# Performance work log

Hardware: AMD Instinct MI355X
Metric: run time of the kernel (lower is better)

The kernel has to match this reference:

```python
import jax, jax.numpy as jnp
import numpy as np

B, L, E = 4, 1024, 1024
H = 16
HD = E // H
CLIP = 16
SCALE = 1.0 / np.sqrt(HD)


def setup_inputs() -> dict:
    key = jax.random.key(0)
    ks = jax.random.split(key, 13)
    def lin(k, fan_in, fan_out, gain):
        # xavier_uniform
        limit = gain * np.sqrt(6.0 / (fan_in + fan_out))
        return jax.random.uniform(k, (fan_out, fan_in), jnp.float32, -limit, limit)
    inv_sqrt2 = 1.0 / np.sqrt(2.0)
    return {
        "query": jax.random.normal(ks[0], (B, L, E), jnp.float32),
        "key": jax.random.normal(ks[1], (B, L, E), jnp.float32),
        "value": jax.random.normal(ks[2], (B, L, E), jnp.float32),
        "wq": lin(ks[3], E, E, inv_sqrt2), "bq": jnp.zeros((E,), jnp.float32),
        "wk": lin(ks[4], E, E, inv_sqrt2), "bk": jnp.zeros((E,), jnp.float32),
        "wv": lin(ks[5], E, E, inv_sqrt2), "bv": jnp.zeros((E,), jnp.float32),
        "wo": lin(ks[6], E, E, 1.0), "bo": jnp.zeros((E,), jnp.float32),
        "rel_k": jax.random.normal(ks[7], (2 * CLIP + 1, HD), jnp.float32) * 0.02,
        "rel_v": jax.random.normal(ks[8], (2 * CLIP + 1, HD), jnp.float32) * 0.02,
    }


def _heads(x):  # (B, L, E) -> (B, H, L, HD)
    return x.reshape(B, L, H, HD).transpose(0, 2, 1, 3)


def reference(query, key, value, wq, bq, wk, bk, wv, bv, wo, bo, rel_k, rel_v):
    q = _heads(query @ wq.T + bq)
    k = _heads(key @ wk.T + bk)
    v = _heads(value @ wv.T + bv)

    # relative-position index matrix (L_q, L_k), clipped to [-CLIP, CLIP]
    pos = jnp.arange(L)
    dist = jnp.clip(pos[None, :] - pos[:, None], -CLIP, CLIP) + CLIP
    r_k = rel_k[dist]  # (L, L, HD)
    r_v = rel_v[dist]  # (L, L, HD)

    dot = jnp.einsum('bhid,bhjd->bhij', q, k)
    rel = jnp.einsum('bhid,ijd->bhij', q, r_k)
    scores = (dot + rel) * SCALE
    attn = jax.nn.softmax(scores, axis=-1)

    y = jnp.einsum('bhij,bhjd->bhid', attn, v) + jnp.einsum('bhij,ijd->bhid', attn, r_v)
    y = y.transpose(0, 2, 1, 3).reshape(B, L, E)
    return y @ wo.T + bo
```

## Files before the change

### kernel.cpp

```cpp
#include <hip/hip_runtime.h>

#define BB 4
#define LL 1024
#define EE 1024
#define HH 16
#define HD 64
#define NBUCKET 33
#define SCALE 0.125f
#define SC2 (0.125f * 1.44269504088896f)

typedef unsigned short u16;
using f32x4 = __attribute__((ext_vector_type(4))) float;
using s16x8 = __attribute__((ext_vector_type(8))) short;

__device__ __forceinline__ u16 f2bf(float f) {
  union { float f; unsigned u; } x; x.f = f;
  unsigned r = (x.u + 0x7fffu + ((x.u >> 16) & 1u)) >> 16;
  return (u16)r;
}

__device__ __forceinline__ void gld_lds16(const void* g, void* s) {
  __builtin_amdgcn_global_load_lds((const __attribute__((address_space(1))) void*)g,
                                   (__attribute__((address_space(3))) void*)s, 16, 0, 0);
}

__global__ __launch_bounds__(256) void cvt_w(
    const float* __restrict__ wq, const float* __restrict__ wk, const float* __restrict__ wv,
    const float* __restrict__ wo, const float* __restrict__ rk,
    u16* __restrict__ owq, u16* __restrict__ owk, u16* __restrict__ owv,
    u16* __restrict__ owo, u16* __restrict__ ork) {
  const int bid = blockIdx.x;
  const int tid = threadIdx.x;
  if (bid < 4096) {
    const int z = bid >> 10;
    const int i = (bid & 1023) * 256 + tid;
    const float* in = z == 0 ? wq : (z == 1 ? wk : (z == 2 ? wv : wo));
    u16* out = z == 0 ? owq : (z == 1 ? owk : (z == 2 ? owv : owo));
    float4 f = ((const float4*)in)[i];
    ushort4 o;
    o.x = f2bf(f.x); o.y = f2bf(f.y); o.z = f2bf(f.z); o.w = f2bf(f.w);
    ((ushort4*)out)[i] = o;
  } else {
    const int i = (bid - 4096) * 256 + tid;
    ork[i] = (i < 33 * 64) ? f2bf(rk[i]) : (u16)0;
  }
}

template <int MODE>
__device__ __forceinline__ void gemm128_f32a(const float* __restrict__ A,
                                             const u16* __restrict__ Bw,
                                             const float* __restrict__ bias,
                                             u16* __restrict__ obf,
                                             int M, int N, int K, int m0, int n0) {
  __shared__ u16 a_sm[128 * 64];
  __shared__ u16 b_sm[128 * 64];
  const int tid = threadIdx.x;
  const int wave = tid >> 6, lane = tid & 63;
  const int row16 = lane & 15, quad = lane >> 4;
  const int wr = (wave >> 1) * 64, wc = (wave & 1) * 64;
  const int srow = lane >> 3, scol = (lane & 7) * 8;

  f32x4 acc[4][4] = {};

  for (int k0 = 0; k0 < K; k0 += 64) {
#pragma unroll
    for (int t = 0; t < 4; ++t) {
      const int chunk = wave * 4 + t;
      const int r = chunk * 8 + srow;
      gld_lds16(Bw + (size_t)(n0 + r) * K + k0 + scol, b_sm + chunk * 512);
    }
#pragma unroll
    for (int p = 0; p < 4; ++p) {
      const int pc = p * 256 + tid;
      const int r = pc >> 3, c0 = (pc & 7) * 8;
      const float4* src = (const float4*)(A + (size_t)(m0 + r) * K + k0 + c0);
      const float4 f0 = src[0], f1 = src[1];
      unsigned w0, w1, w2, w3;
      asm("v_cvt_pk_bf16_f32 %0, %1, %2" : "=v"(w0) : "v"(f0.x), "v"(f0.y));
      asm("v_cvt_pk_bf16_f32 %0, %1, %2" : "=v"(w1) : "v"(f0.z), "v"(f0.w));
      asm("v_cvt_pk_bf16_f32 %0, %1, %2" : "=v"(w2) : "v"(f1.x), "v"(f1.y));
      asm("v_cvt_pk_bf16_f32 %0, %1, %2" : "=v"(w3) : "v"(f1.z), "v"(f1.w));
      union { unsigned u[4]; s16x8 v; } w;
      w.u[0] = w0; w.u[1] = w1; w.u[2] = w2; w.u[3] = w3;
      *(s16x8*)&a_sm[r * 64 + c0] = w.v;
    }
    __syncthreads();
#pragma unroll
    for (int ks = 0; ks < 2; ++ks) {
      s16x8 af[4], bf[4];
#pragma unroll
      for (int mi = 0; mi < 4; ++mi)
        af[mi] = *(const s16x8*)&a_sm[(wr + mi * 16 + row16) * 64 + ks * 32 + quad * 8];
#pragma unroll
      for (int ni = 0; ni < 4; ++ni)
        bf[ni] = *(const s16x8*)&b_sm[(wc + ni * 16 + row16) * 64 + ks * 32 + quad * 8];
#pragma unroll
      for (int mi = 0; mi < 4; ++mi)
#pragma unroll
        for (int ni = 0; ni < 4; ++ni)
          acc[mi][ni] = __builtin_amdgcn_mfma_f32_16x16x32_bf16(af[mi], bf[ni], acc[mi][ni], 0, 0, 0);
    }
    __syncthreads();
  }

#pragma unroll
  for (int mi = 0; mi < 4; ++mi)
#pragma unroll
    for (int ni = 0; ni < 4; ++ni) {
      const int n = n0 + wc + ni * 16 + row16;
      const float bn = bias[n];
      if (MODE == 2) {
        const int mr0 = m0 + wr + mi * 16 + quad * 4;
        const int b = mr0 >> 10, l = mr0 & 1023;
        const int h = n >> 6, hd = n & 63;
        ushort4 o;
        o.x = f2bf(acc[mi][ni][0] + bn);
        o.y = f2bf(acc[mi][ni][1] + bn);
        o.z = f2bf(acc[mi][ni][2] + bn);
        o.w = f2bf(acc[mi][ni][3] + bn);
        *(ushort4*)&obf[((size_t)((b * HH + h) * HD + hd)) * LL + l] = o;
      } else {
#pragma unroll
        for (int r = 0; r < 4; ++r) {
          const int m = m0 + wr + mi * 16 + quad * 4 + r;
          const float v = acc[mi][ni][r] + bn;
          const int b = m >> 10, l = m & 1023, h = n >> 6, hd = n & 63;
          obf[((size_t)((b * HH + h) * LL + l)) * HD + hd] = f2bf(v);
        }
      }
    }
}

__device__ __forceinline__ void gemm128_bt_f32out(const u16* __restrict__ A,
                                                  const u16* __restrict__ Bw,
                                                  const float* __restrict__ bias,
                                                  float* __restrict__ ofp,
                                                  int M, int N, int K, int m0, int n0) {
  __shared__ u16 a_sm[128 * 64];
  __shared__ u16 b_sm[128 * 64];
  const int tid = threadIdx.x;
  const int wave = tid >> 6, lane = tid & 63;
  const int row16 = lane & 15, quad = lane >> 4;
  const int wr = (wave >> 1) * 64, wc = (wave & 1) * 64;
  const int srow = lane >> 3, scol = (lane & 7) * 8;

  f32x4 acc[4][4] = {};

  for (int k0 = 0; k0 < K; k0 += 64) {
#pragma unroll
    for (int t = 0; t < 4; ++t) {
      const int chunk = wave * 4 + t;
      const int r = chunk * 8 + srow;
      gld_lds16(A + (size_t)(m0 + r) * K + k0 + scol, a_sm + chunk * 512);
      gld_lds16(Bw + (size_t)(n0 + r) * K + k0 + scol, b_sm + chunk * 512);
    }
    __syncthreads();
#pragma unroll
    for (int ks = 0; ks < 2; ++ks) {
      s16x8 af[4], bf[4];
#pragma unroll
      for (int mi = 0; mi < 4; ++mi)
        af[mi] = *(const s16x8*)&a_sm[(wr + mi * 16 + row16) * 64 + ks * 32 + quad * 8];
#pragma unroll
      for (int ni = 0; ni < 4; ++ni)
        bf[ni] = *(const s16x8*)&b_sm[(wc + ni * 16 + row16) * 64 + ks * 32 + quad * 8];
#pragma unroll
      for (int mi = 0; mi < 4; ++mi)
#pragma unroll
        for (int ni = 0; ni < 4; ++ni)
          acc[mi][ni] = __builtin_amdgcn_mfma_f32_16x16x32_bf16(af[mi], bf[ni], acc[mi][ni], 0, 0, 0);
    }
    __syncthreads();
  }

#pragma unroll
  for (int mi = 0; mi < 4; ++mi)
#pragma unroll
    for (int ni = 0; ni < 4; ++ni) {
      const int n = n0 + wc + ni * 16 + row16;
      const float bn = bias[n];
#pragma unroll
      for (int r = 0; r < 4; ++r) {
        const int m = m0 + wr + mi * 16 + quad * 4 + r;
        ofp[(size_t)m * N + n] = acc[mi][ni][r] + bn;
      }
    }
}

__global__ __launch_bounds__(256) void proj_gemm(
    const float* __restrict__ xq, const float* __restrict__ xk, const float* __restrict__ xv,
    const u16* __restrict__ wqb, const u16* __restrict__ wkb, const u16* __restrict__ wvb,
    const float* __restrict__ bq, const float* __restrict__ bk, const float* __restrict__ bv,
    u16* __restrict__ oq, u16* __restrict__ ok, u16* __restrict__ ovt) {
  if (blockIdx.z == 0)
    gemm128_f32a<0>(xq, wqb, bq, oq, BB * LL, EE, EE, blockIdx.y * 128, blockIdx.x * 128);
  else if (blockIdx.z == 1)
    gemm128_f32a<0>(xk, wkb, bk, ok, BB * LL, EE, EE, blockIdx.y * 128, blockIdx.x * 128);
  else
    gemm128_f32a<2>(xv, wvb, bv, ovt, BB * LL, EE, EE, blockIdx.y * 128, blockIdx.x * 128);
}

__global__ __launch_bounds__(256) void out_gemm(const u16* __restrict__ Y,
                                                const u16* __restrict__ wob,
                                                const float* __restrict__ bo,
                                                float* __restrict__ out) {
  gemm128_bt_f32out(Y, wob, bo, out, BB * LL, EE, EE, blockIdx.y * 128, blockIdx.x * 128);
}

__global__ __launch_bounds__(256) void attn_fused(
    const u16* __restrict__ Q, const u16* __restrict__ Kb, const u16* __restrict__ Vt,
    const u16* __restrict__ RKp, const float* __restrict__ RV, u16* __restrict__ Y) {
  __shared__ __align__(16) float qr_sm[4][576];
  __shared__ __align__(16) float s_sm[4][16 * 36];
  __shared__ __align__(16) unsigned char kv[16384];

  const int tid = threadIdx.x;
  const int wave = tid >> 6, lane = tid & 63;
  const int row16 = lane & 15, quad = lane >> 4;
  const int bh = blockIdx.x & 63;
  const int i0 = (blockIdx.x >> 6) * 64;
  const int wq0 = i0 + wave * 16;
  const u16* qp = Q + (size_t)bh * LL * HD;
  const char* kpB = (const char*)(Kb + (size_t)bh * LL * HD);
  const char* vpB = (const char*)(Vt + (size_t)bh * HD * LL);

  float* qr_w = &qr_sm[wave][0];
  float* s_w = &s_sm[wave][0];

  int srcK[2], srcV[2];
#pragma unroll
  for (int t = 0; t < 2; ++t) {
    const int cK = (wave * 2 + t) * 64 + lane;
    const int rw = cK >> 3;
    const int cb = ((cK * 16) & 127) ^ ((rw & 7) << 4);
    srcK[t] = rw * 128 + cb;
    srcV[t] = rw * 2048 + cb;
  }
  const int q2 = row16 >> 2;
  const int prow = ((((q2 << 1) | (q2 >> 1)) & 3) << 2) + (row16 & 3);
  const int swzK = (prow & 7) << 4;
  const int swzV = (row16 & 7) << 4;
  const int rho4 = (((quad << 1) | (quad >> 1)) & 3) << 2;

#pragma unroll
  for (int t = 0; t < 2; ++t) {
    gld_lds16(kpB + srcK[t], kv + (wave * 2 + t) * 1024);
    gld_lds16(vpB + srcV[t], kv + 8192 + (wave * 2 + t) * 1024);
  }

  for (int t = lane; t < 16 * 36; t += 64) s_w[t] = 0.f;

  s16x8 qf[2];
#pragma unroll
  for (int ks = 0; ks < 2; ++ks)
    qf[ks] = *(const s16x8*)(qp + (size_t)(wq0 + row16) * HD + ks * 32 + quad * 8);

  f32x4 a0, a2;
#pragma unroll
  for (int nt = 0; nt < 3; ++nt) {
    f32x4 a = {};
#pragma unroll
    for (int ks = 0; ks < 2; ++ks) {
      s16x8 afr = *(const s16x8*)(RKp + (size_t)(nt * 16 + row16) * HD + ks * 32 + quad * 8);
      a = __builtin_amdgcn_mfma_f32_16x16x32_bf16(afr, qf[ks], a, 0, 0, 0);
    }
    if (nt == 0) a0 = a;
    if (nt == 2) a2 = a;
#pragma unroll
    for (int r = 0; r < 4; ++r) {
      const int bk = nt * 16 + quad * 4 + r;
      if (bk < NBUCKET) qr_w[bk * 17 + row16] = a[r];
    }
  }
  const float blo = __shfl(a0[0], row16);
  const float bhi = __shfl(a2[0], row16);

  f32x4 oacc[4] = {};
  float rsum = 0.f, plos = 0.f, phis = 0.f;
  int baseg[4];
#pragma unroll
  for (int g = 0; g < 4; ++g) baseg[g] = g * 16 + rho4 - wq0 - row16;

  for (int jt = 0; jt < 16; ++jt) {
    const int j0 = jt * 64;
    if (jt) {
#pragma unroll
      for (int t = 0; t < 2; ++t) {
        gld_lds16(kpB + (size_t)j0 * 128 + srcK[t], kv + (wave * 2 + t) * 1024);
        gld_lds16(vpB + (size_t)j0 * 2 + srcV[t], kv + 8192 + (wave * 2 + t) * 1024);
      }
    }
    asm volatile("s_waitcnt vmcnt(0)" ::: "memory");
    __builtin_amdgcn_s_barrier();
    __builtin_amdgcn_sched_barrier(0);

    f32x4 sacc[4] = {};
#pragma unroll
    for (int ks = 0; ks < 2; ++ks)
#pragma unroll
      for (int g = 0; g < 4; ++g) {
        const int L = (g * 16 + prow) * 128 + ks * 64 + quad * 16;
        const s16x8 kfr = *(const s16x8*)(kv + (L ^ swzK));
        sacc[g] = __builtin_amdgcn_mfma_f32_16x16x32_bf16(kfr, qf[ks], sacc[g], 0, 0, 0);
      }

    unsigned pk[4][2];
    const bool far_lo = (wq0 >= j0 + 79);
    const bool far_hi = (j0 >= wq0 + 31);
    if (far_lo || far_hi) {
      const float bb = (far_lo ? blo : bhi) * SC2;
      float tacc = 0.f;
#pragma unroll
      for (int g = 0; g < 4; ++g)
#pragma unroll
        for (int rr = 0; rr < 2; ++rr) {
          const float pv0 = __builtin_amdgcn_exp2f(sacc[g][rr * 2] * SC2 + bb);
          const float pv1 = __builtin_amdgcn_exp2f(sacc[g][rr * 2 + 1] * SC2 + bb);
          tacc += pv0 + pv1;
          unsigned c;
          asm("v_cvt_pk_bf16_f32 %0, %1, %2" : "=v"(c) : "v"(pv0), "v"(pv1));
          pk[g][rr] = c;
        }
      rsum += tacc;
      if (far_lo) plos += tacc; else phis += tacc;
    } else {
#pragma unroll
      for (int g = 0; g < 4; ++g)
#pragma unroll
        for (int rr = 0; rr < 2; ++rr) {
          float pv2[2];
#pragma unroll
          for (int e = 0; e < 2; ++e) {
            const int r = rr * 2 + e;
            const int dr = baseg[g] + j0 + r;
            int bk = dr < -16 ? -16 : (dr > 16 ? 16 : dr);
            bk += 16;
            const float bias = qr_w[bk * 17 + row16];
            const float pv = __builtin_amdgcn_exp2f((sacc[g][r] + bias) * SC2);
            pv2[e] = pv;
            rsum += pv;
            if (dr <= -16) plos += pv;
            else if (dr >= 16) phis += pv;
            else atomicAdd(&s_w[row16 * 36 + bk], pv);
          }
          unsigned c;
          asm("v_cvt_pk_bf16_f32 %0, %1, %2" : "=v"(c) : "v"(pv2[0]), "v"(pv2[1]));
          pk[g][rr] = c;
        }
    }

    s16x8 pf[2];
#pragma unroll
    for (int ks = 0; ks < 2; ++ks) {
      unsigned x0 = pk[ks * 2][0], y0 = pk[ks * 2 + 1][0];
      unsigned x1 = pk[ks * 2][1], y1 = pk[ks * 2 + 1][1];
      asm("v_permlane32_swap_b32 %0, %1" : "+v"(x0), "+v"(y0));
      asm("v_permlane32_swap_b32 %0, %1" : "+v"(x1), "+v"(y1));
      union { unsigned u[4]; s16x8 v; } pfu;
      pfu.u[0] = x0; pfu.u[1] = x1; pfu.u[2] = y0; pfu.u[3] = y1;
      pf[ks] = pfu.v;
    }

#pragma unroll
    for (int ks = 0; ks < 2; ++ks)
#pragma unroll
      for (int dt = 0; dt < 4; ++dt) {
        const int L = (dt * 16 + row16) * 128 + ks * 64 + quad * 16;
        const s16x8 vfr = *(const s16x8*)(kv + 8192 + (L ^ swzV));
        oacc[dt] = __builtin_amdgcn_mfma_f32_16x16x32_bf16(vfr, pf[ks], oacc[dt], 0, 0, 0);
      }

    asm volatile("s_waitcnt lgkmcnt(0)" ::: "memory");
    __builtin_amdgcn_s_barrier();
    __builtin_amdgcn_sched_barrier(0);
  }

  float t1 = rsum + __shfl_xor(rsum, 16);
  const float lacc = t1 + __shfl_xor(t1, 32);
  t1 = plos + __shfl_xor(plos, 16);
  const float slo = t1 + __shfl_xor(t1, 32);
  t1 = phis + __shfl_xor(phis, 16);
  const float shi = t1 + __shfl_xor(t1, 32);

  float* rv_sm = (float*)kv;
  for (int t = tid; t < NBUCKET * HD; t += 256) rv_sm[t] = RV[t];
  __syncthreads();

  const int b = bh >> 4, h = bh & 15;
  float rel[4][4] = {};
  for (int bk = 0; bk < NBUCKET; ++bk) {
    float sv = s_w[row16 * 36 + bk];
    if (bk == 0) sv += slo;
    if (bk == 32) sv += shi;
#pragma unroll
    for (int dt = 0; dt < 4; ++dt) {
      const f32x4 rv4 = *(const f32x4*)&rv_sm[bk * HD + dt * 16 + quad * 4];
#pragma unroll
      for (int r = 0; r < 4; ++r) rel[dt][r] += sv * rv4[r];
    }
  }
  const float inv = 1.0f / lacc;
#pragma unroll
  for (int dt = 0; dt < 4; ++dt) {
    ushort4 o;
    o.x = f2bf((oacc[dt][0] + rel[dt][0]) * inv);
    o.y = f2bf((oacc[dt][1] + rel[dt][1]) * inv);
    o.z = f2bf((oacc[dt][2] + rel[dt][2]) * inv);
    o.w = f2bf((oacc[dt][3] + rel[dt][3]) * inv);
    *(ushort4*)&Y[((size_t)(b * LL + wq0 + row16)) * EE + h * HD + dt * 16 + quad * 4] = o;
  }
}

extern "C" void kernel_launch(void* const* d_in, const int* in_sizes, int n_in,
                              void* d_out, int out_size, void* d_ws, size_t ws_size,
                              hipStream_t stream) {
  const float* query = (const float*)d_in[0];
  const float* key_  = (const float*)d_in[1];
  const float* value = (const float*)d_in[2];
  const float* wq = (const float*)d_in[3];
  const float* bq = (const float*)d_in[4];
  const float* wk = (const float*)d_in[5];
  const float* bk = (const float*)d_in[6];
  const float* wv = (const float*)d_in[7];
  const float* bv = (const float*)d_in[8];
  const float* wo = (const float*)d_in[9];
  const float* bo = (const float*)d_in[10];
  const float* rel_k = (const float*)d_in[11];
  const float* rel_v = (const float*)d_in[12];

  char* base = (char*)d_ws;
  size_t off = 0;
  auto alloc = [&](size_t bytes) -> void* {
    void* p = base + off;
    off += (bytes + 255) & ~(size_t)255;
    return p;
  };
  const size_t XE = (size_t)BB * LL * EE;
  u16* wqb   = (u16*)alloc((size_t)EE * EE * 2);
  u16* wkb   = (u16*)alloc((size_t)EE * EE * 2);
  u16* wvb   = (u16*)alloc((size_t)EE * EE * 2);
  u16* wob   = (u16*)alloc((size_t)EE * EE * 2);
  u16* q_ws  = (u16*)alloc(XE * 2);
  u16* k_ws  = (u16*)alloc(XE * 2);
  u16* vt_ws = (u16*)alloc(XE * 2);
  u16* relkp = (u16*)alloc(48 * 64 * 2);
  u16* y_ws  = (u16*)alloc(XE * 2);

  cvt_w<<<4108, 256, 0, stream>>>(wq, wk, wv, wo, rel_k, wqb, wkb, wvb, wob, relkp);

  proj_gemm<<<dim3(EE / 128, BB * LL / 128, 3), 256, 0, stream>>>(
      query, key_, value, wqb, wkb, wvb, bq, bk, bv, q_ws, k_ws, vt_ws);

  attn_fused<<<1024, 256, 0, stream>>>(q_ws, k_ws, vt_ws, relkp, rel_v, y_ws);

  out_gemm<<<dim3(EE / 128, BB * LL / 128), 256, 0, stream>>>(y_ws, wob, bo, (float*)d_out);
}
```

Measured before the change: 261.2 us.

## Swizzle GEMM LDS tiles and remap block order for XCD locality

```diff
diff --git a/kernel.cpp b/kernel.cpp
--- a/kernel.cpp
+++ b/kernel.cpp
@@ -47,18 +47,18 @@
 }
 
 template <int MODE>
-__device__ __forceinline__ void gemm128_f32a(const float* __restrict__ A,
+__device__ __forceinline__ void gemm128_f32a(u16* a_sm, u16* b_sm,
+                                             const float* __restrict__ A,
                                              const u16* __restrict__ Bw,
                                              const float* __restrict__ bias,
                                              u16* __restrict__ obf,
                                              int M, int N, int K, int m0, int n0) {
-  __shared__ u16 a_sm[128 * 64];
-  __shared__ u16 b_sm[128 * 64];
   const int tid = threadIdx.x;
   const int wave = tid >> 6, lane = tid & 63;
   const int row16 = lane & 15, quad = lane >> 4;
   const int wr = (wave >> 1) * 64, wc = (wave & 1) * 64;
   const int srow = lane >> 3, scol = (lane & 7) * 8;
+  const int rsw = (row16 & 7) * 8;
 
   f32x4 acc[4][4] = {};
 
@@ -67,7 +67,8 @@
     for (int t = 0; t < 4; ++t) {
       const int chunk = wave * 4 + t;
       const int r = chunk * 8 + srow;
-      gld_lds16(Bw + (size_t)(n0 + r) * K + k0 + scol, b_sm + chunk * 512);
+      const int cs = scol ^ ((r & 7) * 8);
+      gld_lds16(Bw + (size_t)(n0 + r) * K + k0 + cs, b_sm + chunk * 512);
     }
 #pragma unroll
     for (int p = 0; p < 4; ++p) {
@@ -82,18 +83,19 @@
       asm("v_cvt_pk_bf16_f32 %0, %1, %2" : "=v"(w3) : "v"(f1.z), "v"(f1.w));
       union { unsigned u[4]; s16x8 v; } w;
       w.u[0] = w0; w.u[1] = w1; w.u[2] = w2; w.u[3] = w3;
-      *(s16x8*)&a_sm[r * 64 + c0] = w.v;
+      *(s16x8*)&a_sm[r * 64 + (c0 ^ ((r & 7) * 8))] = w.v;
     }
     __syncthreads();
 #pragma unroll
     for (int ks = 0; ks < 2; ++ks) {
+      const int cfs = (ks * 32 + quad * 8) ^ rsw;
       s16x8 af[4], bf[4];
 #pragma unroll
       for (int mi = 0; mi < 4; ++mi)
-        af[mi] = *(const s16x8*)&a_sm[(wr + mi * 16 + row16) * 64 + ks * 32 + quad * 8];
+        af[mi] = *(const s16x8*)&a_sm[(wr + mi * 16 + row16) * 64 + cfs];
 #pragma unroll
       for (int ni = 0; ni < 4; ++ni)
-        bf[ni] = *(const s16x8*)&b_sm[(wc + ni * 16 + row16) * 64 + ks * 32 + quad * 8];
+        bf[ni] = *(const s16x8*)&b_sm[(wc + ni * 16 + row16) * 64 + cfs];
 #pragma unroll
       for (int mi = 0; mi < 4; ++mi)
 #pragma unroll
@@ -131,18 +133,42 @@
     }
 }
 
-__device__ __forceinline__ void gemm128_bt_f32out(const u16* __restrict__ A,
-                                                  const u16* __restrict__ Bw,
-                                                  const float* __restrict__ bias,
-                                                  float* __restrict__ ofp,
-                                                  int M, int N, int K, int m0, int n0) {
+__global__ __launch_bounds__(256) void proj_gemm(
+    const float* __restrict__ xq, const float* __restrict__ xk, const float* __restrict__ xv,
+    const u16* __restrict__ wqb, const u16* __restrict__ wkb, const u16* __restrict__ wvb,
+    const float* __restrict__ bq, const float* __restrict__ bk, const float* __restrict__ bv,
+    u16* __restrict__ oq, u16* __restrict__ ok, u16* __restrict__ ovt) {
   __shared__ u16 a_sm[128 * 64];
   __shared__ u16 b_sm[128 * 64];
+  const int work = (blockIdx.x & 7) * 96 + (blockIdx.x >> 3);
+  const int z = work >> 8;
+  const int m0 = ((work & 255) >> 3) * 128;
+  const int n0 = (work & 7) * 128;
+  if (z == 0)
+    gemm128_f32a<0>(a_sm, b_sm, xq, wqb, bq, oq, BB * LL, EE, EE, m0, n0);
+  else if (z == 1)
+    gemm128_f32a<0>(a_sm, b_sm, xk, wkb, bk, ok, BB * LL, EE, EE, m0, n0);
+  else
+    gemm128_f32a<2>(a_sm, b_sm, xv, wvb, bv, ovt, BB * LL, EE, EE, m0, n0);
+}
+
+__global__ __launch_bounds__(256) void out_gemm(const u16* __restrict__ A,
+                                                const u16* __restrict__ Bw,
+                                                const float* __restrict__ bias,
+                                                float* __restrict__ ofp) {
+  __shared__ u16 a_sm[128 * 64];
+  __shared__ u16 b_sm[128 * 64];
+  const int work = (blockIdx.x & 7) * 32 + (blockIdx.x >> 3);
+  const int m0 = (work >> 3) * 128;
+  const int n0 = (work & 7) * 128;
+  const int N = EE, K = EE;
+
   const int tid = threadIdx.x;
   const int wave = tid >> 6, lane = tid & 63;
   const int row16 = lane & 15, quad = lane >> 4;
   const int wr = (wave >> 1) * 64, wc = (wave & 1) * 64;
   const int srow = lane >> 3, scol = (lane & 7) * 8;
+  const int rsw = (row16 & 7) * 8;
 
   f32x4 acc[4][4] = {};
 
@@ -151,19 +177,21 @@
     for (int t = 0; t < 4; ++t) {
       const int chunk = wave * 4 + t;
       const int r = chunk * 8 + srow;
-      gld_lds16(A + (size_t)(m0 + r) * K + k0 + scol, a_sm + chunk * 512);
-      gld_lds16(Bw + (size_t)(n0 + r) * K + k0 + scol, b_sm + chunk * 512);
+      const int cs = scol ^ ((r & 7) * 8);
+      gld_lds16(A + (size_t)(m0 + r) * K + k0 + cs, a_sm + chunk * 512);
+      gld_lds16(Bw + (size_t)(n0 + r) * K + k0 + cs, b_sm + chunk * 512);
     }
     __syncthreads();
 #pragma unroll
     for (int ks = 0; ks < 2; ++ks) {
+      const int cfs = (ks * 32 + quad * 8) ^ rsw;
       s16x8 af[4], bf[4];
 #pragma unroll
       for (int mi = 0; mi < 4; ++mi)
-        af[mi] = *(const s16x8*)&a_sm[(wr + mi * 16 + row16) * 64 + ks * 32 + quad * 8];
+        af[mi] = *(const s16x8*)&a_sm[(wr + mi * 16 + row16) * 64 + cfs];
 #pragma unroll
       for (int ni = 0; ni < 4; ++ni)
-        bf[ni] = *(const s16x8*)&b_sm[(wc + ni * 16 + row16) * 64 + ks * 32 + quad * 8];
+        bf[ni] = *(const s16x8*)&b_sm[(wc + ni * 16 + row16) * 64 + cfs];
 #pragma unroll
       for (int mi = 0; mi < 4; ++mi)
 #pragma unroll
@@ -185,26 +213,6 @@
         ofp[(size_t)m * N + n] = acc[mi][ni][r] + bn;
       }
     }
-}
-
-__global__ __launch_bounds__(256) void proj_gemm(
-    const float* __restrict__ xq, const float* __restrict__ xk, const float* __restrict__ xv,
-    const u16* __restrict__ wqb, const u16* __restrict__ wkb, const u16* __restrict__ wvb,
-    const float* __restrict__ bq, const float* __restrict__ bk, const float* __restrict__ bv,
-    u16* __restrict__ oq, u16* __restrict__ ok, u16* __restrict__ ovt) {
-  if (blockIdx.z == 0)
-    gemm128_f32a<0>(xq, wqb, bq, oq, BB * LL, EE, EE, blockIdx.y * 128, blockIdx.x * 128);
-  else if (blockIdx.z == 1)
-    gemm128_f32a<0>(xk, wkb, bk, ok, BB * LL, EE, EE, blockIdx.y * 128, blockIdx.x * 128);
-  else
-    gemm128_f32a<2>(xv, wvb, bv, ovt, BB * LL, EE, EE, blockIdx.y * 128, blockIdx.x * 128);
-}
-
-__global__ __launch_bounds__(256) void out_gemm(const u16* __restrict__ Y,
-                                                const u16* __restrict__ wob,
-                                                const float* __restrict__ bo,
-                                                float* __restrict__ out) {
-  gemm128_bt_f32out(Y, wob, bo, out, BB * LL, EE, EE, blockIdx.y * 128, blockIdx.x * 128);
 }
 
 __global__ __launch_bounds__(256) void attn_fused(
@@ -448,10 +456,10 @@
 
   cvt_w<<<4108, 256, 0, stream>>>(wq, wk, wv, wo, rel_k, wqb, wkb, wvb, wob, relkp);
 
-  proj_gemm<<<dim3(EE / 128, BB * LL / 128, 3), 256, 0, stream>>>(
+  proj_gemm<<<768, 256, 0, stream>>>(
       query, key_, value, wqb, wkb, wvb, bq, bk, bv, q_ws, k_ws, vt_ws);
 
   attn_fused<<<1024, 256, 0, stream>>>(q_ws, k_ws, vt_ws, relkp, rel_v, y_ws);
 
-  out_gemm<<<dim3(EE / 128, BB * LL / 128), 256, 0, stream>>>(y_ws, wob, bo, (float*)d_out);
-}
+  out_gemm<<<256, 256, 0, stream>>>(y_ws, wob, bo, (float*)d_out);
+}
```

Result: faster. 251.2 us (-3.8%).
